# Kernel tuning notes

Hardware: AMD Instinct MI355X
Metric: run time of the kernel (lower is better)

## Reference

```python
import jax, jax.numpy as jnp
import numpy as np

B, N, NFEAT = 32, 512, 256
NHID, NHEADS, NOUT = 64, 8, 128
ALPHA = 0.2    # GraphAttn LeakyReLU slope
ACVT_SLOPE = 0.01  # default nn.LeakyReLU slope in GAT.acvt
EPS = 1e-12


def _leaky(x, slope):
    return jnp.where(x >= 0, x, slope * x)


def setup_inputs() -> dict:
    key = jax.random.key(0)
    ks = jax.random.split(key, 10)
    s = lambda fan_in: 1.0 / np.sqrt(fan_in)
    return {
        "batch_descs": jax.random.normal(ks[0], (B, N, NFEAT), dtype=jnp.float32),
        # per-head GraphAttn params (nn.Linear weights, no bias)
        "W_tran": jax.random.uniform(ks[1], (NHEADS, NHID, NFEAT), jnp.float32, -s(NFEAT), s(NFEAT)),
        "a1": jax.random.uniform(ks[2], (NHEADS, NHID), jnp.float32, -s(NHID), s(NHID)),
        "a2": jax.random.uniform(ks[3], (NHEADS, NHID), jnp.float32, -s(NHID), s(NHID)),
        # output GraphAttn: in = NHID*NHEADS, out = NOUT
        "W_out": jax.random.uniform(ks[4], (NOUT, NHID * NHEADS), jnp.float32, -s(NHID * NHEADS), s(NHID * NHEADS)),
        "a1_out": jax.random.uniform(ks[5], (NOUT,), jnp.float32, -s(NOUT), s(NOUT)),
        "a2_out": jax.random.uniform(ks[6], (NOUT,), jnp.float32, -s(NOUT), s(NOUT)),
        # final nn.Linear(nout, nout) with bias
        "W_lin": jax.random.uniform(ks[7], (NOUT, NOUT), jnp.float32, -s(NOUT), s(NOUT)),
        "b_lin": jax.random.uniform(ks[8], (NOUT,), jnp.float32, -s(NOUT), s(NOUT)),
    }


def reference(batch_descs, W_tran, a1, a2, W_out, a1_out, a2_out, W_lin, b_lin):
    def gat_one_object(x):  # x: [N, NFEAT]; dense all-ones adj (ignored by GraphAttn)
        # ---- multi-head GraphAttn ----
        h = jnp.einsum('nf,hdf->hnd', x, W_tran)          # [H, N, NHID]
        e1 = jnp.einsum('hnd,hd->hn', h, a1)              # [H, N]
        e2 = jnp.einsum('hnd,hd->hn', h, a2)              # [H, N]
        # e[h, j, k] = a1(h_k) + a2(h_j); softmax over k (torch dim=1 on [N,N])
        e = _leaky(e1[:, None, :] + e2[:, :, None], ALPHA)  # [H, N, N]
        att = jax.nn.softmax(e, axis=-1)
        o = jnp.einsum('hjk,hkd->hjd', att, h)            # [H, N, NHID]
        o = jnp.transpose(o, (1, 0, 2)).reshape(N, NHEADS * NHID)  # concat heads
        # ---- acvt (dropout2 is identity in eval) ----
        x2 = _leaky(o, ACVT_SLOPE)
        # ---- output GraphAttn ----
        h2 = x2 @ W_out.T                                 # [N, NOUT]
        f1 = h2 @ a1_out                                  # [N]
        f2 = h2 @ a2_out                                  # [N]
        e_o = _leaky(f1[None, :] + f2[:, None], ALPHA)    # [N, N]
        att_o = jax.nn.softmax(e_o, axis=-1)
        out = att_o @ h2                                  # [N, NOUT]
        out = jnp.mean(out, axis=0)                       # [NOUT]
        return out @ W_lin.T + b_lin

    feats = jax.vmap(gat_one_object)(batch_descs)         # [B, NOUT]
    # F.normalize(p=2, dim=-1) with eps clamp
    norm = jnp.maximum(jnp.linalg.norm(feats, axis=-1, keepdims=True), EPS)
    return feats / norm
```

## Files before the change

kernel.cpp:

```cpp
#include <hip/hip_runtime.h>
#include <hip/hip_bf16.h>
#include <math.h>

#define ALPHA 0.2f
#define ACVT 0.01f

typedef __attribute__((ext_vector_type(8))) __bf16 bf16x8;
typedef __attribute__((ext_vector_type(4))) __bf16 bf16x4;
typedef __attribute__((ext_vector_type(4))) float f32x4;

__device__ __forceinline__ bf16x8 cvt8(const float* p) {
    float4 v0 = *(const float4*)p;
    float4 v1 = *(const float4*)(p + 4);
    bf16x8 o;
    o[0] = (__bf16)v0.x; o[1] = (__bf16)v0.y; o[2] = (__bf16)v0.z; o[3] = (__bf16)v0.w;
    o[4] = (__bf16)v1.x; o[5] = (__bf16)v1.y; o[6] = (__bf16)v1.z; o[7] = (__bf16)v1.w;
    return o;
}

__global__ __launch_bounds__(256) void gemm1_f(
    const float* __restrict__ X, const float* __restrict__ Wt,
    __bf16* __restrict__ HT,
    const float* __restrict__ a1, const float* __restrict__ a2,
    float* __restrict__ E1, float* __restrict__ E2) {
    __shared__ char As[128 * 128];
    __shared__ char Bs[128 * 128];
    __shared__ char Tt[128 * 264];
    const int tid = threadIdx.x;
    const int w = tid >> 6, lane = tid & 63;
    const int wm = w >> 1, wn = w & 1;
    const int r = lane & 15, g = lane >> 4;
    const int L = blockIdx.x;
    const int W = (L & 7) * 64 + (L >> 3);
    const int m_tile = W >> 2, n_tile = W & 3;
    const int m0 = m_tile * 128;
    const int n0 = n_tile * 128;

    f32x4 acc[4][4];
#pragma unroll
    for (int mt = 0; mt < 4; ++mt)
#pragma unroll
        for (int nt = 0; nt < 4; ++nt) {
            acc[mt][nt][0] = 0.f; acc[mt][nt][1] = 0.f;
            acc[mt][nt][2] = 0.f; acc[mt][nt][3] = 0.f;
        }

    const int sr = tid >> 3;
    const int c8 = (tid & 7) * 8;

    for (int k0 = 0; k0 < 256; k0 += 64) {
        __syncthreads();
#pragma unroll
        for (int i = 0; i < 4; ++i) {
            int row = sr + i * 32;
            bf16x8 va = cvt8(X + (size_t)(m0 + row) * 256 + k0 + c8);
            *(bf16x8*)(As + row * 128 + ((c8 * 2) ^ ((row & 7) << 4))) = va;
            bf16x8 vb = cvt8(Wt + (size_t)(n0 + row) * 256 + k0 + c8);
            *(bf16x8*)(Bs + row * 128 + ((c8 * 2) ^ ((row & 7) << 4))) = vb;
        }
        __syncthreads();
#pragma unroll
        for (int kk = 0; kk < 64; kk += 32) {
            bf16x8 af[4], bfv[4];
#pragma unroll
            for (int mt = 0; mt < 4; ++mt) {
                int row = wm * 64 + mt * 16 + r;
                af[mt] = *(const bf16x8*)(As + row * 128 +
                                          (((kk + g * 8) * 2) ^ ((row & 7) << 4)));
            }
#pragma unroll
            for (int nt = 0; nt < 4; ++nt) {
                int row = wn * 64 + nt * 16 + r;
                bfv[nt] = *(const bf16x8*)(Bs + row * 128 +
                                           (((kk + g * 8) * 2) ^ ((row & 7) << 4)));
            }
#pragma unroll
            for (int mt = 0; mt < 4; ++mt)
#pragma unroll
                for (int nt = 0; nt < 4; ++nt)
                    acc[mt][nt] = __builtin_amdgcn_mfma_f32_16x16x32_bf16(
                        af[mt], bfv[nt], acc[mt][nt], 0, 0, 0);
        }
    }

#pragma unroll
    for (int mt = 0; mt < 4; ++mt) {
        int node = wm * 64 + mt * 16 + g * 4;
#pragma unroll
        for (int nt = 0; nt < 4; ++nt) {
            int d_blk = wn * 64 + nt * 16 + r;
            bf16x4 pv;
#pragma unroll
            for (int reg = 0; reg < 4; ++reg) pv[reg] = (__bf16)acc[mt][nt][reg];
            *(bf16x4*)(Tt + d_blk * 264 + node * 2) = pv;
        }
    }
    __syncthreads();
    {
        const int b = m0 >> 9, nn = m0 & 511;
        const int h0 = n_tile * 2;
#pragma unroll
        for (int i = 0; i < 8; ++i) {
            int d_row = (tid >> 4) + i * 16;
            int hrow = (b * 8 + h0 + (d_row >> 6)) * 64 + (d_row & 63);
            bf16x8 v = *(const bf16x8*)(Tt + d_row * 264 + (tid & 15) * 16);
            *(bf16x8*)(HT + (size_t)hrow * 512 + nn + (tid & 15) * 8) = v;
        }
    }
    const int h = n_tile * 2 + wn;
    float w1[4], w2[4];
#pragma unroll
    for (int nt = 0; nt < 4; ++nt) {
        w1[nt] = a1[h * 64 + nt * 16 + r];
        w2[nt] = a2[h * 64 + nt * 16 + r];
    }
#pragma unroll
    for (int mt = 0; mt < 4; ++mt)
#pragma unroll
        for (int reg = 0; reg < 4; ++reg) {
            float s1 = 0.f, s2 = 0.f;
#pragma unroll
            for (int nt = 0; nt < 4; ++nt) {
                s1 += acc[mt][nt][reg] * w1[nt];
                s2 += acc[mt][nt][reg] * w2[nt];
            }
#pragma unroll
            for (int off = 1; off <= 8; off <<= 1) {
                s1 += __shfl_xor(s1, off, 64);
                s2 += __shfl_xor(s2, off, 64);
            }
            if (r == 0) {
                int m = m0 + wm * 64 + mt * 16 + g * 4 + reg;
                int b = m >> 9, n = m & 511;
                E1[(size_t)(b * 8 + h) * 512 + n] = s1;
                E2[(size_t)(b * 8 + h) * 512 + n] = s2;
            }
        }
}

__global__ __launch_bounds__(256) void attn_s(const __bf16* __restrict__ HT,
                                              const float* __restrict__ E1,
                                              const float* __restrict__ E2,
                                              __bf16* __restrict__ OL) {
    __shared__ char Hc0[4096];
    __shared__ char Hc1[4096];
    __shared__ float e1s[512];
    __shared__ float redm[256];
    __shared__ float zrow[4][32];
    __shared__ float e1maxS;

    const int bid = blockIdx.x;
    const int bh = bid >> 2, qq = bid & 3;
    const int b = bh >> 3, h = bh & 7;
    const int tid = threadIdx.x;
    const int w = tid >> 6, lane = tid & 63;
    const int r = lane & 15, g = lane >> 4;

    for (int i = tid; i < 512; i += 256) e1s[i] = E1[(size_t)bh * 512 + i];
    __syncthreads();
    redm[tid] = fmaxf(e1s[tid], e1s[tid + 256]);
    __syncthreads();
    if (tid < 64) {
        float m = fmaxf(fmaxf(redm[tid], redm[tid + 64]),
                        fmaxf(redm[tid + 128], redm[tid + 192]));
#pragma unroll
        for (int off = 32; off >= 1; off >>= 1) m = fmaxf(m, __shfl_xor(m, off, 64));
        if (tid == 0) e1maxS = m;
    }
    __syncthreads();
    const float e1max = e1maxS;

    float ee2[2], mm[2];
    const float* e2g = E2 + (size_t)bh * 512 + qq * 128 + w * 32;
#pragma unroll
    for (int mt = 0; mt < 2; ++mt) {
        float v = e2g[mt * 16 + r];
        ee2[mt] = v;
        float s = e1max + v;
        mm[mt] = fmaxf(s, ALPHA * s);
    }

    f32x4 acc[2][4];
#pragma unroll
    for (int mt = 0; mt < 2; ++mt)
#pragma unroll
        for (int nt = 0; nt < 4; ++nt) {
            acc[mt][nt][0] = 0.f; acc[mt][nt][1] = 0.f;
            acc[mt][nt][2] = 0.f; acc[mt][nt][3] = 0.f;
        }
    float zac[2] = {0.f, 0.f};

    const int d_s = tid >> 2, kq = tid & 3;
    const __bf16* hsrc = HT + (size_t)(bh * 64 + d_s) * 512 + kq * 8;
    const int lwo = d_s * 64 + ((kq * 16) ^ ((d_s & 3) << 4));
    char* cur = Hc0;
    char* nxt = Hc1;
    *(bf16x8*)(cur + lwo) = *(const bf16x8*)hsrc;
    __syncthreads();

    for (int c = 0; c < 16; ++c) {
        bf16x8 stg;
        if (c < 15) stg = *(const bf16x8*)(hsrc + (c + 1) * 32);

        const float* ep = e1s + c * 32 + g * 8;
        float4 ea = *(const float4*)(ep);
        float4 eb = *(const float4*)(ep + 4);
        float e1c[8] = {ea.x, ea.y, ea.z, ea.w, eb.x, eb.y, eb.z, eb.w};

        bf16x8 bfr[4];
#pragma unroll
        for (int nt = 0; nt < 4; ++nt) {
            int d = nt * 16 + r;
            bfr[nt] = *(const bf16x8*)(cur + d * 64 + ((g * 16) ^ ((d & 3) << 4)));
        }
#pragma unroll
        for (int mt = 0; mt < 2; ++mt) {
            bf16x8 af;
            float zp = 0.f;
#pragma unroll
            for (int q = 0; q < 8; ++q) {
                float s = e1c[q] + ee2[mt];
                s = fmaxf(s, ALPHA * s);
                float p = __expf(s - mm[mt]);
                zp += p;
                af[q] = (__bf16)p;
            }
            zac[mt] += zp;
#pragma unroll
            for (int nt = 0; nt < 4; ++nt)
                acc[mt][nt] =
                    __builtin_amdgcn_mfma_f32_16x16x32_bf16(af, bfr[nt], acc[mt][nt], 0, 0, 0);
        }

        if (c < 15) *(bf16x8*)(nxt + lwo) = stg;
        __syncthreads();
        char* t = cur; cur = nxt; nxt = t;
    }

#pragma unroll
    for (int mt = 0; mt < 2; ++mt) {
        float z = zac[mt];
        z += __shfl_xor(z, 16, 64);
        z += __shfl_xor(z, 32, 64);
        if (g == 0) zrow[w][mt * 16 + r] = 1.f / z;
    }

    __bf16* ob = OL + ((size_t)b * 512 + qq * 128 + w * 32) * 512 + h * 64;
#pragma unroll
    for (int mt = 0; mt < 2; ++mt) {
#pragma unroll
        for (int reg = 0; reg < 4; ++reg) {
            int row = mt * 16 + g * 4 + reg;
            float zi = zrow[w][row];
#pragma unroll
            for (int nt = 0; nt < 4; ++nt) {
                float v = acc[mt][nt][reg] * zi;
                v = fmaxf(v, ACVT * v);
                ob[(size_t)row * 512 + nt * 16 + r] = (__bf16)v;
            }
        }
    }
}

__global__ __launch_bounds__(256) void gemm2_f(
    const __bf16* __restrict__ OL, const float* __restrict__ Wo,
    __bf16* __restrict__ H2,
    const float* __restrict__ a1o, const float* __restrict__ a2o,
    float* __restrict__ F1, float* __restrict__ F2) {
    __shared__ char As[32 * 128];
    __shared__ char Bs[128 * 128];
    __shared__ float fred[2][32][2];
    const int tid = threadIdx.x;
    const int w = tid >> 6, lane = tid & 63;
    const int wm = w >> 1, wn = w & 1;
    const int r = lane & 15, g = lane >> 4;
    const int m0 = blockIdx.x * 32;

    f32x4 acc[4];
#pragma unroll
    for (int nt = 0; nt < 4; ++nt) {
        acc[nt][0] = 0.f; acc[nt][1] = 0.f; acc[nt][2] = 0.f; acc[nt][3] = 0.f;
    }

    const int sra = tid >> 3;
    const int c8 = (tid & 7) * 8;

    for (int k0 = 0; k0 < 512; k0 += 64) {
        __syncthreads();
        {
            bf16x8 va = *(const bf16x8*)((const char*)OL +
                                         ((size_t)(m0 + sra) * 512 + k0) * 2 + c8 * 2);
            *(bf16x8*)(As + sra * 128 + ((c8 * 2) ^ ((sra & 7) << 4))) = va;
        }
#pragma unroll
        for (int i = 0; i < 4; ++i) {
            int row = sra + i * 32;
            bf16x8 vb = cvt8(Wo + (size_t)row * 512 + k0 + c8);
            *(bf16x8*)(Bs + row * 128 + ((c8 * 2) ^ ((row & 7) << 4))) = vb;
        }
        __syncthreads();
#pragma unroll
        for (int kk = 0; kk < 64; kk += 32) {
            int arow = wm * 16 + r;
            bf16x8 af = *(const bf16x8*)(As + arow * 128 +
                                         (((kk + g * 8) * 2) ^ ((arow & 7) << 4)));
            bf16x8 bfv[4];
#pragma unroll
            for (int nt = 0; nt < 4; ++nt) {
                int row = wn * 64 + nt * 16 + r;
                bfv[nt] = *(const bf16x8*)(Bs + row * 128 +
                                           (((kk + g * 8) * 2) ^ ((row & 7) << 4)));
            }
#pragma unroll
            for (int nt = 0; nt < 4; ++nt)
                acc[nt] = __builtin_amdgcn_mfma_f32_16x16x32_bf16(af, bfv[nt], acc[nt], 0, 0, 0);
        }
    }

#pragma unroll
    for (int reg = 0; reg < 4; ++reg) {
        int row = m0 + wm * 16 + g * 4 + reg;
#pragma unroll
        for (int nt = 0; nt < 4; ++nt)
            H2[(size_t)row * 128 + wn * 64 + nt * 16 + r] = (__bf16)acc[nt][reg];
    }
    float w1[4], w2[4];
#pragma unroll
    for (int nt = 0; nt < 4; ++nt) {
        w1[nt] = a1o[wn * 64 + nt * 16 + r];
        w2[nt] = a2o[wn * 64 + nt * 16 + r];
    }
#pragma unroll
    for (int reg = 0; reg < 4; ++reg) {
        float s1 = 0.f, s2 = 0.f;
#pragma unroll
        for (int nt = 0; nt < 4; ++nt) {
            s1 += acc[nt][reg] * w1[nt];
            s2 += acc[nt][reg] * w2[nt];
        }
#pragma unroll
        for (int off = 1; off <= 8; off <<= 1) {
            s1 += __shfl_xor(s1, off, 64);
            s2 += __shfl_xor(s2, off, 64);
        }
        if (r == 0) {
            int lr = wm * 16 + g * 4 + reg;
            fred[wn][lr][0] = s1;
            fred[wn][lr][1] = s2;
        }
    }
    __syncthreads();
    if (tid < 32) {
        int m = m0 + tid;
        int b = m >> 9, n = m & 511;
        F1[(size_t)b * 512 + n] = fred[0][tid][0] + fred[1][tid][0];
        F2[(size_t)b * 512 + n] = fred[0][tid][1] + fred[1][tid][1];
    }
}

__global__ __launch_bounds__(256) void zw_k(const float* __restrict__ F1,
                                            const float* __restrict__ F2,
                                            float* __restrict__ WP) {
    __shared__ float f1s[512];
    __shared__ float wpart[4][512];
    __shared__ float redm[256];
    const int b = blockIdx.x >> 4, jc = blockIdx.x & 15;
    const int tid = threadIdx.x;
    const int w = tid >> 6, lane = tid & 63;

    f1s[tid] = F1[(size_t)b * 512 + tid];
    f1s[tid + 256] = F1[(size_t)b * 512 + tid + 256];
#pragma unroll
    for (int i = 0; i < 8; ++i) wpart[w][lane + 64 * i] = 0.f;
    __syncthreads();
    redm[tid] = fmaxf(f1s[tid], f1s[tid + 256]);
    __syncthreads();
    if (tid < 64) {
        float m = fmaxf(fmaxf(redm[tid], redm[tid + 64]), fmaxf(redm[tid + 128], redm[tid + 192]));
#pragma unroll
        for (int off = 32; off >= 1; off >>= 1) m = fmaxf(m, __shfl_xor(m, off, 64));
        if (tid == 0) redm[0] = m;
    }
    __syncthreads();
    const float f1m = redm[0];

    for (int jj = 0; jj < 8; ++jj) {
        int j = jc * 32 + w * 8 + jj;
        float f2j = F2[(size_t)b * 512 + j];
        float sj = f1m + f2j;
        float mj = fmaxf(sj, ALPHA * sj);
        float pv[8];
        float z = 0.f;
#pragma unroll
        for (int i = 0; i < 8; ++i) {
            float s = f1s[lane + 64 * i] + f2j;
            s = fmaxf(s, ALPHA * s);
            float p = __expf(s - mj);
            pv[i] = p;
            z += p;
        }
#pragma unroll
        for (int off = 32; off >= 1; off >>= 1) z += __shfl_xor(z, off, 64);
        float inv = 1.f / z;
#pragma unroll
        for (int i = 0; i < 8; ++i) wpart[w][lane + 64 * i] += pv[i] * inv;
    }
    __syncthreads();
    for (int i = tid; i < 512; i += 256)
        WP[(size_t)(b * 16 + jc) * 512 + i] =
            wpart[0][i] + wpart[1][i] + wpart[2][i] + wpart[3][i];
}

__global__ __launch_bounds__(512) void finalv_k(const float* __restrict__ WP,
                                                const __bf16* __restrict__ H2,
                                                const float* __restrict__ Wl,
                                                const float* __restrict__ bl,
                                                float* __restrict__ out) {
    __shared__ float wsL[512];
    __shared__ float part[4][128];
    __shared__ float vs[128];
    __shared__ float fo_s[128];
    __shared__ float r0;
    const int b = blockIdx.x, tid = threadIdx.x;
    {
        float s = 0.f;
#pragma unroll
        for (int jc = 0; jc < 16; ++jc) s += WP[(size_t)(b * 16 + jc) * 512 + tid];
        wsL[tid] = s;
    }
    __syncthreads();
    {
        const int q = tid >> 7, d = tid & 127;
        const __bf16* h2p = H2 + ((size_t)b * 512 + q * 128) * 128 + d;
        float acc = 0.f;
#pragma unroll 8
        for (int i = 0; i < 128; ++i) acc += wsL[q * 128 + i] * (float)h2p[(size_t)i * 128];
        part[q][d] = acc;
    }
    __syncthreads();
    if (tid < 128)
        vs[tid] = (part[0][tid] + part[1][tid] + part[2][tid] + part[3][tid]) * (1.f / 512.f);
    __syncthreads();
    if (tid < 128) {
        float fo = bl[tid];
        const float* wl = Wl + (size_t)tid * 128;
#pragma unroll 4
        for (int d = 0; d < 128; d += 4)
            fo += vs[d] * wl[d] + vs[d + 1] * wl[d + 1] + vs[d + 2] * wl[d + 2] +
                  vs[d + 3] * wl[d + 3];
        fo_s[tid] = fo;
    }
    __syncthreads();
    if (tid < 64) {
        float s = fo_s[tid] * fo_s[tid] + fo_s[tid + 64] * fo_s[tid + 64];
#pragma unroll
        for (int off = 32; off >= 1; off >>= 1) s += __shfl_xor(s, off, 64);
        if (tid == 0) r0 = s;
    }
    __syncthreads();
    float inv = 1.f / fmaxf(sqrtf(r0), 1e-12f);
    if (tid < 128) out[(size_t)b * 128 + tid] = fo_s[tid] * inv;
}

extern "C" void kernel_launch(void* const* d_in, const int* in_sizes, int n_in,
                              void* d_out, int out_size, void* d_ws, size_t ws_size,
                              hipStream_t stream) {
    const float* X = (const float*)d_in[0];
    const float* Wt = (const float*)d_in[1];
    const float* a1 = (const float*)d_in[2];
    const float* a2 = (const float*)d_in[3];
    const float* Wo = (const float*)d_in[4];
    const float* a1o = (const float*)d_in[5];
    const float* a2o = (const float*)d_in[6];
    const float* Wl = (const float*)d_in[7];
    const float* bl = (const float*)d_in[8];
    float* out = (float*)d_out;

    char* p = (char*)d_ws;
    __bf16* HT = (__bf16*)p;  p += (size_t)8388608 * 2;
    __bf16* OL = (__bf16*)p;  p += (size_t)8388608 * 2;
    float* E1 = (float*)p;    p += (size_t)131072 * 4;
    float* E2 = (float*)p;    p += (size_t)131072 * 4;
    __bf16* H2 = (__bf16*)p;  p += (size_t)2097152 * 2;
    float* F1 = (float*)p;    p += (size_t)16384 * 4;
    float* F2 = (float*)p;    p += (size_t)16384 * 4;
    float* WP = (float*)p;    p += (size_t)262144 * 4;

    gemm1_f<<<512, 256, 0, stream>>>(X, Wt, HT, a1, a2, E1, E2);
    attn_s<<<1024, 256, 0, stream>>>(HT, E1, E2, OL);
    gemm2_f<<<512, 256, 0, stream>>>(OL, Wo, H2, a1o, a2o, F1, F2);
    zw_k<<<512, 256, 0, stream>>>(F1, F2, WP);
    finalv_k<<<32, 512, 0, stream>>>(WP, H2, Wl, bl, out);
}
```

Baseline: 142.2 us.

## Eliminate second GEMM by folding attention vectors and reassociating output projection

The output-layer GEMM (OL @ Wo^T) is removed. The attention kernel now computes per-head partial f1/f2 scores by projecting a1o/a2o through Wo (Wo^T a), and these partials are summed across heads in zw_k. The final kernel reassociates mean(att @ OL @ Wo^T) as ((w^T OL) @ Wo^T), reading OL directly instead of H2. This drops a full kernel and the H2 round trip. In exchange, every attention block recomputes the small Wo^T a projections, and the final kernel does a 512x512 matvec per batch in only 32 blocks, which may serialise.

```diff
diff --git a/kernel.cpp b/kernel.cpp
--- a/kernel.cpp
+++ b/kernel.cpp
@@ -138,16 +138,19 @@
         }
 }
 
-__global__ __launch_bounds__(256) void attn_s(const __bf16* __restrict__ HT,
-                                              const float* __restrict__ E1,
-                                              const float* __restrict__ E2,
-                                              __bf16* __restrict__ OL) {
+__global__ __launch_bounds__(256) void attn_s(
+    const __bf16* __restrict__ HT, const float* __restrict__ E1,
+    const float* __restrict__ E2, const float* __restrict__ Wo,
+    const float* __restrict__ a1o, const float* __restrict__ a2o,
+    __bf16* __restrict__ OL, float* __restrict__ F1P, float* __restrict__ F2P) {
     __shared__ char Hc0[4096];
     __shared__ char Hc1[4096];
     __shared__ float e1s[512];
     __shared__ float redm[256];
     __shared__ float zrow[4][32];
     __shared__ float e1maxS;
+    __shared__ float atp[2][4][64];
+    __shared__ float at1[64], at2[64];
 
     const int bid = blockIdx.x;
     const int bh = bid >> 2, qq = bid & 3;
@@ -156,9 +159,28 @@
     const int w = tid >> 6, lane = tid & 63;
     const int r = lane & 15, g = lane >> 4;
 
+    {
+        const int d = tid & 63, part = tid >> 6;
+        const float* wop = Wo + (size_t)(part * 32) * 512 + h * 64 + d;
+        float p1 = 0.f, p2 = 0.f;
+#pragma unroll 8
+        for (int c = 0; c < 32; ++c) {
+            float wv = wop[(size_t)c * 512];
+            p1 += wv * a1o[part * 32 + c];
+            p2 += wv * a2o[part * 32 + c];
+        }
+        atp[0][part][d] = p1;
+        atp[1][part][d] = p2;
+    }
     for (int i = tid; i < 512; i += 256) e1s[i] = E1[(size_t)bh * 512 + i];
     __syncthreads();
     redm[tid] = fmaxf(e1s[tid], e1s[tid + 256]);
+    if (tid < 64)
+        at1[tid] = atp[0][0][tid] + atp[0][1][tid] + atp[0][2][tid] + atp[0][3][tid];
+    else if (tid < 128) {
+        int d = tid - 64;
+        at2[d] = atp[1][0][d] + atp[1][1][d] + atp[1][2][d] + atp[1][3][d];
+    }
     __syncthreads();
     if (tid < 64) {
         float m = fmaxf(fmaxf(redm[tid], redm[tid + 64]),
@@ -245,6 +267,12 @@
         if (g == 0) zrow[w][mt * 16 + r] = 1.f / z;
     }
 
+    float aa1[4], aa2[4];
+#pragma unroll
+    for (int nt = 0; nt < 4; ++nt) {
+        aa1[nt] = at1[nt * 16 + r];
+        aa2[nt] = at2[nt * 16 + r];
+    }
     __bf16* ob = OL + ((size_t)b * 512 + qq * 128 + w * 32) * 512 + h * 64;
 #pragma unroll
     for (int mt = 0; mt < 2; ++mt) {
@@ -252,124 +280,49 @@
         for (int reg = 0; reg < 4; ++reg) {
             int row = mt * 16 + g * 4 + reg;
             float zi = zrow[w][row];
+            float s1 = 0.f, s2 = 0.f;
 #pragma unroll
             for (int nt = 0; nt < 4; ++nt) {
                 float v = acc[mt][nt][reg] * zi;
                 v = fmaxf(v, ACVT * v);
                 ob[(size_t)row * 512 + nt * 16 + r] = (__bf16)v;
-            }
-        }
-    }
-}
-
-__global__ __launch_bounds__(256) void gemm2_f(
-    const __bf16* __restrict__ OL, const float* __restrict__ Wo,
-    __bf16* __restrict__ H2,
-    const float* __restrict__ a1o, const float* __restrict__ a2o,
-    float* __restrict__ F1, float* __restrict__ F2) {
-    __shared__ char As[32 * 128];
-    __shared__ char Bs[128 * 128];
-    __shared__ float fred[2][32][2];
-    const int tid = threadIdx.x;
-    const int w = tid >> 6, lane = tid & 63;
-    const int wm = w >> 1, wn = w & 1;
-    const int r = lane & 15, g = lane >> 4;
-    const int m0 = blockIdx.x * 32;
-
-    f32x4 acc[4];
-#pragma unroll
-    for (int nt = 0; nt < 4; ++nt) {
-        acc[nt][0] = 0.f; acc[nt][1] = 0.f; acc[nt][2] = 0.f; acc[nt][3] = 0.f;
-    }
-
-    const int sra = tid >> 3;
-    const int c8 = (tid & 7) * 8;
-
-    for (int k0 = 0; k0 < 512; k0 += 64) {
-        __syncthreads();
-        {
-            bf16x8 va = *(const bf16x8*)((const char*)OL +
-                                         ((size_t)(m0 + sra) * 512 + k0) * 2 + c8 * 2);
-            *(bf16x8*)(As + sra * 128 + ((c8 * 2) ^ ((sra & 7) << 4))) = va;
-        }
-#pragma unroll
-        for (int i = 0; i < 4; ++i) {
-            int row = sra + i * 32;
-            bf16x8 vb = cvt8(Wo + (size_t)row * 512 + k0 + c8);
-            *(bf16x8*)(Bs + row * 128 + ((c8 * 2) ^ ((row & 7) << 4))) = vb;
-        }
-        __syncthreads();
-#pragma unroll
-        for (int kk = 0; kk < 64; kk += 32) {
-            int arow = wm * 16 + r;
-            bf16x8 af = *(const bf16x8*)(As + arow * 128 +
-                                         (((kk + g * 8) * 2) ^ ((arow & 7) << 4)));
-            bf16x8 bfv[4];
-#pragma unroll
-            for (int nt = 0; nt < 4; ++nt) {
-                int row = wn * 64 + nt * 16 + r;
-                bfv[nt] = *(const bf16x8*)(Bs + row * 128 +
-                                           (((kk + g * 8) * 2) ^ ((row & 7) << 4)));
-            }
-#pragma unroll
-            for (int nt = 0; nt < 4; ++nt)
-                acc[nt] = __builtin_amdgcn_mfma_f32_16x16x32_bf16(af, bfv[nt], acc[nt], 0, 0, 0);
-        }
-    }
-
-#pragma unroll
-    for (int reg = 0; reg < 4; ++reg) {
-        int row = m0 + wm * 16 + g * 4 + reg;
-#pragma unroll
-        for (int nt = 0; nt < 4; ++nt)
-            H2[(size_t)row * 128 + wn * 64 + nt * 16 + r] = (__bf16)acc[nt][reg];
-    }
-    float w1[4], w2[4];
-#pragma unroll
-    for (int nt = 0; nt < 4; ++nt) {
-        w1[nt] = a1o[wn * 64 + nt * 16 + r];
-        w2[nt] = a2o[wn * 64 + nt * 16 + r];
-    }
-#pragma unroll
-    for (int reg = 0; reg < 4; ++reg) {
-        float s1 = 0.f, s2 = 0.f;
-#pragma unroll
-        for (int nt = 0; nt < 4; ++nt) {
-            s1 += acc[nt][reg] * w1[nt];
-            s2 += acc[nt][reg] * w2[nt];
-        }
-#pragma unroll
-        for (int off = 1; off <= 8; off <<= 1) {
-            s1 += __shfl_xor(s1, off, 64);
-            s2 += __shfl_xor(s2, off, 64);
-        }
-        if (r == 0) {
-            int lr = wm * 16 + g * 4 + reg;
-            fred[wn][lr][0] = s1;
-            fred[wn][lr][1] = s2;
-        }
-    }
-    __syncthreads();
-    if (tid < 32) {
-        int m = m0 + tid;
-        int b = m >> 9, n = m & 511;
-        F1[(size_t)b * 512 + n] = fred[0][tid][0] + fred[1][tid][0];
-        F2[(size_t)b * 512 + n] = fred[0][tid][1] + fred[1][tid][1];
-    }
-}
-
-__global__ __launch_bounds__(256) void zw_k(const float* __restrict__ F1,
-                                            const float* __restrict__ F2,
+                s1 += v * aa1[nt];
+                s2 += v * aa2[nt];
+            }
+#pragma unroll
+            for (int off = 1; off <= 8; off <<= 1) {
+                s1 += __shfl_xor(s1, off, 64);
+                s2 += __shfl_xor(s2, off, 64);
+            }
+            if (r == 0) {
+                int j = qq * 128 + w * 32 + row;
+                F1P[(size_t)h * 16384 + b * 512 + j] = s1;
+                F2P[(size_t)h * 16384 + b * 512 + j] = s2;
+            }
+        }
+    }
+}
+
+__global__ __launch_bounds__(256) void zw_k(const float* __restrict__ F1P,
+                                            const float* __restrict__ F2P,
                                             float* __restrict__ WP) {
-    __shared__ float f1s[512];
+    __shared__ float f1s[512], f2s[512];
     __shared__ float wpart[4][512];
     __shared__ float redm[256];
     const int b = blockIdx.x >> 4, jc = blockIdx.x & 15;
     const int tid = threadIdx.x;
     const int w = tid >> 6, lane = tid & 63;
 
-    f1s[tid] = F1[(size_t)b * 512 + tid];
-    f1s[tid + 256] = F1[(size_t)b * 512 + tid + 256];
+    for (int i = tid; i < 512; i += 256) {
+        float s1 = 0.f, s2 = 0.f;
+#pragma unroll
+        for (int hh = 0; hh < 8; ++hh) {
+            s1 += F1P[(size_t)hh * 16384 + b * 512 + i];
+            s2 += F2P[(size_t)hh * 16384 + b * 512 + i];
+        }
+        f1s[i] = s1;
+        f2s[i] = s2;
+    }
 #pragma unroll
     for (int i = 0; i < 8; ++i) wpart[w][lane + 64 * i] = 0.f;
     __syncthreads();
@@ -386,7 +339,7 @@
 
     for (int jj = 0; jj < 8; ++jj) {
         int j = jc * 32 + w * 8 + jj;
-        float f2j = F2[(size_t)b * 512 + j];
+        float f2j = f2s[j];
         float sj = f1m + f2j;
         float mj = fmaxf(sj, ALPHA * sj);
         float pv[8];
@@ -411,14 +364,16 @@
             wpart[0][i] + wpart[1][i] + wpart[2][i] + wpart[3][i];
 }
 
-__global__ __launch_bounds__(512) void finalv_k(const float* __restrict__ WP,
-                                                const __bf16* __restrict__ H2,
+__global__ __launch_bounds__(512) void ufinal_k(const float* __restrict__ WP,
+                                                const __bf16* __restrict__ OL,
+                                                const float* __restrict__ Wo,
                                                 const float* __restrict__ Wl,
                                                 const float* __restrict__ bl,
                                                 float* __restrict__ out) {
     __shared__ float wsL[512];
+    __shared__ float us[512];
     __shared__ float part[4][128];
-    __shared__ float vs[128];
+    __shared__ float vfull[128];
     __shared__ float fo_s[128];
     __shared__ float r0;
     const int b = blockIdx.x, tid = threadIdx.x;
@@ -430,24 +385,32 @@
     }
     __syncthreads();
     {
-        const int q = tid >> 7, d = tid & 127;
-        const __bf16* h2p = H2 + ((size_t)b * 512 + q * 128) * 128 + d;
+        const __bf16* olp = OL + (size_t)b * 512 * 512 + tid;
         float acc = 0.f;
 #pragma unroll 8
-        for (int i = 0; i < 128; ++i) acc += wsL[q * 128 + i] * (float)h2p[(size_t)i * 128];
-        part[q][d] = acc;
+        for (int k = 0; k < 512; ++k) acc += wsL[k] * (float)olp[(size_t)k * 512];
+        us[tid] = acc * (1.f / 512.f);
+    }
+    __syncthreads();
+    {
+        const int c = tid & 127, q = tid >> 7;
+        const float* wop = Wo + (size_t)c * 512 + q * 128;
+        float pp = 0.f;
+#pragma unroll 8
+        for (int i = 0; i < 128; ++i) pp += us[q * 128 + i] * wop[i];
+        part[q][c] = pp;
     }
     __syncthreads();
     if (tid < 128)
-        vs[tid] = (part[0][tid] + part[1][tid] + part[2][tid] + part[3][tid]) * (1.f / 512.f);
+        vfull[tid] = part[0][tid] + part[1][tid] + part[2][tid] + part[3][tid];
     __syncthreads();
     if (tid < 128) {
         float fo = bl[tid];
         const float* wl = Wl + (size_t)tid * 128;
 #pragma unroll 4
         for (int d = 0; d < 128; d += 4)
-            fo += vs[d] * wl[d] + vs[d + 1] * wl[d + 1] + vs[d + 2] * wl[d + 2] +
-                  vs[d + 3] * wl[d + 3];
+            fo += vfull[d] * wl[d] + vfull[d + 1] * wl[d + 1] +
+                  vfull[d + 2] * wl[d + 2] + vfull[d + 3] * wl[d + 3];
         fo_s[tid] = fo;
     }
     __syncthreads();
@@ -481,14 +444,12 @@
     __bf16* OL = (__bf16*)p;  p += (size_t)8388608 * 2;
     float* E1 = (float*)p;    p += (size_t)131072 * 4;
     float* E2 = (float*)p;    p += (size_t)131072 * 4;
-    __bf16* H2 = (__bf16*)p;  p += (size_t)2097152 * 2;
-    float* F1 = (float*)p;    p += (size_t)16384 * 4;
-    float* F2 = (float*)p;    p += (size_t)16384 * 4;
+    float* F1P = (float*)p;   p += (size_t)8 * 16384 * 4;
+    float* F2P = (float*)p;   p += (size_t)8 * 16384 * 4;
     float* WP = (float*)p;    p += (size_t)262144 * 4;
 
     gemm1_f<<<512, 256, 0, stream>>>(X, Wt, HT, a1, a2, E1, E2);
-    attn_s<<<1024, 256, 0, stream>>>(HT, E1, E2, OL);
-    gemm2_f<<<512, 256, 0, stream>>>(OL, Wo, H2, a1o, a2o, F1, F2);
-    zw_k<<<512, 256, 0, stream>>>(F1, F2, WP);
-    finalv_k<<<32, 512, 0, stream>>>(WP, H2, Wl, bl, out);
-}
+    attn_s<<<1024, 256, 0, stream>>>(HT, E1, E2, Wo, a1o, a2o, OL, F1P, F2P);
+    zw_k<<<512, 256, 0, stream>>>(F1P, F2P, WP);
+    ufinal_k<<<32, 512, 0, stream>>>(WP, OL, Wo, Wl, bl, out);
+}
```

New measurement: 157.7 us. +10.9%, slower.
